# Kernel tuning notes

Measured on AMD Instinct MI355X. Metric: run time of the kernel, lower is better.

## Reference

```python
import jax, jax.numpy as jnp
import numpy as np

B, K, S = 4096, 32, 6          # batch, n_neighbors, n_shifts
QD, H, NH = 512, 384, 6        # query_dim, hidden_dim, n_heads
HD = H // NH                   # head_dim
NR = 20                        # n_residue_types (table has NR+1 rows)
NBR_IN = S + S + 16 + 1 + 1    # neighbor_proj input dim = 30

def gelu(x):
    return jax.nn.gelu(x, approximate=False)

def setup_inputs():
    key = jax.random.key(0)
    ks = iter(jax.random.split(key, 64))
    def nrm(shape, scale=0.05):
        return jax.random.normal(next(ks), shape, dtype=jnp.float32) * scale
    inp = {}
    inp['query_encoding'] = jax.random.normal(next(ks), (B, QD), dtype=jnp.float32)
    inp['query_residue_code'] = jax.random.randint(next(ks), (B,), 0, NR + 1).astype(jnp.int32)
    inp['query_observed_shifts'] = jax.random.normal(next(ks), (B, S), dtype=jnp.float32)
    inp['query_shift_masks'] = (jax.random.uniform(next(ks), (B, S)) < 0.8).astype(jnp.float32)
    inp['retrieved_shifts'] = jax.random.normal(next(ks), (B, K, S), dtype=jnp.float32)
    inp['retrieved_shift_masks'] = jax.random.uniform(next(ks), (B, K, S)) < 0.8
    inp['retrieved_residue_codes'] = jax.random.randint(next(ks), (B, K), 0, NR + 1).astype(jnp.int32)
    inp['retrieved_distances'] = jax.random.uniform(next(ks), (B, K), dtype=jnp.float32)
    inp['retrieved_valid'] = jax.random.uniform(next(ks), (B, K)) < 0.9
    # parameters (buffers + weights). rc_table kept finite (no NaN rows sampled).
    inp['rc_table'] = nrm((NR + 1, S), 1.0)
    inp['W_qp'] = nrm((QD, H)); inp['b_qp'] = jnp.zeros((H,))
    inp['E_res'] = nrm((NR + 1, 16))
    inp['W_np'] = nrm((NBR_IN, H)); inp['b_np'] = jnp.zeros((H,))
    inp['W_aq'] = nrm((H, H)); inp['b_aq'] = jnp.zeros((H,))
    inp['W_ak'] = nrm((H, H)); inp['b_ak'] = jnp.zeros((H,))
    inp['W_av'] = nrm((H, H)); inp['b_av'] = jnp.zeros((H,))
    inp['W_ss1'] = nrm((2 * S, H // 2)); inp['b_ss1'] = jnp.zeros((H // 2,))
    inp['W_ss2'] = nrm((H // 2, NH)); inp['b_ss2'] = jnp.zeros((NH,))
    inp['W_cp1'] = nrm((H, H)); inp['b_cp1'] = jnp.zeros((H,))
    inp['W_cp2'] = nrm((H, H)); inp['b_cp2'] = jnp.zeros((H,))
    inp['W_sw1'] = nrm((H, H)); inp['b_sw1'] = jnp.zeros((H,))
    inp['W_sw2'] = nrm((H, S)); inp['b_sw2'] = jnp.zeros((S,))
    inp['E_trust'] = nrm((NR + 1, 32))
    inp['W_tq'] = nrm((QD, H)); inp['b_tq'] = jnp.zeros((H,))
    inp['W_tc'] = nrm((H + 32 + 4, H)); inp['b_tc'] = jnp.zeros((H,))
    inp['W_tp1'] = nrm((H + 4, H // 2)); inp['b_tp1'] = jnp.zeros((H // 2,))
    inp['W_tp2'] = nrm((H // 2, 1)); inp['b_tp2'] = jnp.zeros((1,))
    inp['shift_scale'] = jnp.ones((S,)); inp['fallback_shift'] = jnp.zeros((S,))
    inp['fallback_context'] = jnp.zeros((H,))
    return inp

def _forward(p):
    eps = 1e-8
    qcode = p['query_residue_code']; rcodes = p['retrieved_residue_codes']
    smask = p['retrieved_shift_masks']; valid = p['retrieved_valid']
    dist = p['retrieved_distances']; rc = p['rc_table']
    # --- RC correction: corrected = RC[query] + (shift - RC[retrieved]) ---
    qidx = jnp.clip(qcode, 0, rc.shape[0] - 1)
    ridx = jnp.clip(rcodes, 0, rc.shape[0] - 1)
    rc_q = rc[qidx][:, None, :]            # (B,1,S)
    rc_r = rc[ridx]                         # (B,K,S)
    corrected = rc_q + (p['retrieved_shifts'] - rc_r)
    rc_valid = (~jnp.isnan(rc_q)) & (~jnp.isnan(rc_r))
    corrected = jnp.where(rc_valid, corrected, p['retrieved_shifts'])
    shifts = jnp.where(smask, corrected, p['retrieved_shifts'])  # (B,K,S)
    any_valid = valid.any(axis=1)                                # (B,)
    same_type = (rcodes == qcode[:, None]).astype(jnp.float32)   # (B,K)
    # --- projections ---
    q = gelu(p['query_encoding'] @ p['W_qp'] + p['b_qp'])        # (B,H)
    res_emb = p['E_res'][rcodes]                                 # (B,K,16)
    nbr = jnp.concatenate([shifts, smask.astype(jnp.float32), res_emb,
                           dist[..., None], same_type[..., None]], axis=-1)
    kv = gelu(nbr @ p['W_np'] + p['b_np'])                       # (B,K,H)
    # --- multi-head cross attention (single query token) ---
    Qh = (q @ p['W_aq'] + p['b_aq']).reshape(B, NH, HD)
    Kh = (kv @ p['W_ak'] + p['b_ak']).reshape(B, K, NH, HD)
    Vh = (kv @ p['W_av'] + p['b_av']).reshape(B, K, NH, HD)
    scores = jnp.einsum('bhd,bkhd->bhk', Qh, Kh) * (HD ** -0.5)  # (B,NH,K)
    sdiff = jnp.concatenate([
        (p['query_observed_shifts'][:, None, :] - shifts) * p['query_shift_masks'][:, None, :],
        jnp.broadcast_to(p['query_shift_masks'][:, None, :], (B, K, S))], axis=-1)
    bias = gelu(sdiff @ p['W_ss1'] + p['b_ss1']) @ p['W_ss2'] + p['b_ss2']  # (B,K,NH)
    scores = scores + jnp.transpose(bias, (0, 2, 1))
    # if nothing valid, unmask slot 0 (matches torch all_masked fixup)
    valid_eff = valid | ((~any_valid)[:, None] & (jnp.arange(K) == 0)[None, :])
    scores = jnp.where(valid_eff[:, None, :], scores, -10000.0)
    w = jax.nn.softmax(scores, axis=-1)
    attn_out = jnp.einsum('bhk,bkhd->bhd', w, Vh).reshape(B, H)
    ctx = gelu(attn_out @ p['W_cp1'] + p['b_cp1']) @ p['W_cp2'] + p['b_cp2']
    ctx = jnp.where(any_valid[:, None], ctx, p['fallback_context'][None, :])
    # --- shift transfer ---
    swb = gelu(attn_out @ p['W_sw1'] + p['b_sw1']) @ p['W_sw2'] + p['b_sw2']  # (B,S)
    weights = dist[..., None] + same_type[..., None] * 0.5 + swb[:, None, :] * 0.1  # (B,K,S)
    valid_mask = valid[..., None] & smask
    weights = jnp.where(valid_mask, weights, -10000.0)
    weights = jax.nn.softmax(weights, axis=1)
    transferred = jnp.sum(weights * shifts, axis=1) * p['shift_scale']
    transferred = jnp.where(any_valid[:, None], transferred, p['fallback_shift'][None, :])
    # --- trust statistics (no grad in original) ---
    vm = valid_mask.astype(jnp.float32)
    cnt = vm.sum(axis=1)                                         # (B,S)
    cov = cnt / (K + eps)
    mean = (shifts * vm).sum(axis=1) / (cnt + eps)
    var = (((shifts - mean[:, None, :]) ** 2) * vm).sum(axis=1) / (cnt + eps)
    var_n = jnp.clip(jnp.log1p(var), 0.0, 5.0) / 5.0
    mdist = (dist[..., None] * vm).sum(axis=1) / (cnt + eps)
    stp = (same_type[..., None] * vm).sum(axis=1) / (cnt + eps)
    per_stats = jax.lax.stop_gradient(jnp.stack([cov, var_n, mdist, stp], axis=-1))  # (B,S,4)
    vf = valid.astype(jnp.float32)
    n_valid = vf.sum(axis=1, keepdims=True) / K
    n_same = (same_type * vf).sum(axis=1, keepdims=True) / K
    dmask = jnp.where(valid, dist, 0.0)
    gmean = dmask.sum(axis=1, keepdims=True) / (vf.sum(axis=1, keepdims=True) + eps)
    gmax = dmask.max(axis=1, keepdims=True)
    gstats = jax.lax.stop_gradient(jnp.concatenate([gmean, gmax, n_valid, n_same], axis=-1))  # (B,4)
    # --- trust head ---
    qre = p['E_trust'][qcode]                                    # (B,32)
    tq = gelu(p['query_encoding'] @ p['W_tq'] + p['b_tq'])
    tc = gelu(jnp.concatenate([tq, qre, gstats], axis=-1) @ p['W_tc'] + p['b_tc'])  # (B,H)
    tin = jnp.concatenate([jnp.broadcast_to(tc[:, None, :], (B, S, H)), per_stats], axis=-1)
    trust = jax.nn.sigmoid(gelu(tin @ p['W_tp1'] + p['b_tp1']) @ p['W_tp2'] + p['b_tp2'])[..., 0]
    return ctx, transferred, trust

def reference(query_encoding, query_residue_code, query_observed_shifts, query_shift_masks,
              retrieved_shifts, retrieved_shift_masks, retrieved_residue_codes,
              retrieved_distances, retrieved_valid, rc_table,
              W_qp, b_qp, E_res, W_np, b_np, W_aq, b_aq, W_ak, b_ak, W_av, b_av,
              W_ss1, b_ss1, W_ss2, b_ss2, W_cp1, b_cp1, W_cp2, b_cp2,
              W_sw1, b_sw1, W_sw2, b_sw2, E_trust, W_tq, b_tq, W_tc, b_tc,
              W_tp1, b_tp1, W_tp2, b_tp2, shift_scale, fallback_shift, fallback_context):
    return _forward(dict(locals()))
```

## Files before the change

kernel.cpp:

```cpp
#include <hip/hip_runtime.h>

typedef unsigned short u16;
typedef unsigned int u32;
typedef __attribute__((ext_vector_type(8))) short bf16x8;
typedef __attribute__((ext_vector_type(4))) float f32x4;

__device__ __forceinline__ float fs(float f) {
    return (f == f && fabsf(f) < 1e30f) ? f : 0.f;
}
__device__ __forceinline__ float fin(float v) {
    return (v == v && fabsf(v) < 1e30f) ? v : 555.0f;
}
__device__ __forceinline__ u16 f2b(float f) {
    union { float f; unsigned int i; } w; w.f = f;
    unsigned int r = w.i + 0x7FFFu + ((w.i >> 16) & 1u);
    return (u16)(r >> 16);
}
__device__ __forceinline__ float b2f(u16 b) {
    union { unsigned int i; float f; } w; w.i = ((unsigned int)b) << 16;
    return w.f;
}
__device__ __forceinline__ float gelu_f(float x) {
    return 0.5f * x * (1.0f + erff(x * 0.70710678118654752440f));
}

__global__ void fill_kernel(float* __restrict__ out, int n, float val) {
    int i = blockIdx.x * 256 + threadIdx.x;
    if (i < n) out[i] = val;
}

struct CvtSrcs { const float* p[13]; };

__global__ void k_cvt_all(CvtSrcs sp, u16* __restrict__ w) {
    int id = blockIdx.x * 256 + threadIdx.x;
    if (id >= 3634304) return;
    if (id < 2097152) { w[id] = f2b(fs(sp.p[0][id])); return; }
    if (id >= 2637824 && id < 2785280) { w[id] = f2b(fs(sp.p[4][id - 2637824])); return; }
    const float* src; int local, K, N, Kp;
    if (id < 2293760)      { src = sp.p[1];  local = id - 2097152; K = 512; N = 384; Kp = 512; }
    else if (id < 2490368) { src = sp.p[2];  local = id - 2293760; K = 512; N = 384; Kp = 512; }
    else if (id < 2637824) { src = sp.p[3];  local = id - 2490368; K = 384; N = 384; Kp = 384; }
    else if (id < 2932736) { src = sp.p[5];  local = id - 2785280; K = 384; N = 384; Kp = 384; }
    else if (id < 3080192) { src = sp.p[6];  local = id - 2932736; K = 384; N = 384; Kp = 384; }
    else if (id < 3227648) { src = sp.p[7];  local = id - 3080192; K = 384; N = 384; Kp = 384; }
    else if (id < 3375104) { src = sp.p[8];  local = id - 3227648; K = 384; N = 384; Kp = 384; }
    else if (id < 3547136) { src = sp.p[9];  local = id - 3375104; K = 420; N = 384; Kp = 448; }
    else if (id < 3620864) { src = sp.p[10]; local = id - 3547136; K = 384; N = 192; Kp = 384; }
    else if (id < 3633152) { src = sp.p[11]; local = id - 3620864; K = 30;  N = 384; Kp = 32;  }
    else                   { src = sp.p[12]; local = id - 3633152; K = 192; N = 6;   Kp = 192; }
    int n = local / Kp, k = local - n * Kp;
    w[id] = (k < K) ? f2b(fs(src[(size_t)k * N + n])) : (u16)0;
}

__global__ void k_prep(const float* __restrict__ qobs, const float* __restrict__ qmask,
                       const float* __restrict__ rshift, const int* __restrict__ rsmask,
                       const int* __restrict__ qcode, const int* __restrict__ rcodes,
                       const float* __restrict__ rdist, const float* __restrict__ rc_table,
                       const float* __restrict__ E_res,
                       float* __restrict__ nbr, float* __restrict__ sdiff, int NBc)
{
    int gk = blockIdx.x * 256 + threadIdx.x;
    if (gk >= NBc) return;
    int b = gk >> 5;
    int qc = qcode[b], rc = rcodes[gk];
    int qi = min(max(qc, 0), 20), ri = min(max(rc, 0), 20);
    float dist = fs(rdist[gk]);
    float same = (rc == qc) ? 1.f : 0.f;
    float* nr = nbr + (size_t)gk * 30;
    float* sd = sdiff + (size_t)gk * 12;
    for (int s = 0; s < 6; s++) {
        float rs = fs(rshift[gk * 6 + s]);
        bool m = rsmask[gk * 6 + s] != 0;
        float rq = rc_table[qi * 6 + s];
        float rr = rc_table[ri * 6 + s];
        bool rcv = (rq == rq) && (rr == rr) && fabsf(rq) < 1e30f && fabsf(rr) < 1e30f;
        float sh = (m && rcv) ? (rq + rs - rr) : rs;
        nr[s] = sh;
        nr[6 + s] = m ? 1.f : 0.f;
        float qm = fs(qmask[b * 6 + s]);
        sd[s] = (fs(qobs[b * 6 + s]) - sh) * qm;
        sd[6 + s] = qm;
    }
    for (int j = 0; j < 16; j++) nr[12 + j] = fs(E_res[ri * 16 + j]);
    nr[28] = dist;
    nr[29] = same;
}

__global__ void k_stats_w(const float* __restrict__ nbr, const int* __restrict__ rvalid,
                          float* __restrict__ pst, float* __restrict__ gst,
                          float* __restrict__ anyv, int BCc)
{
    int wid = (blockIdx.x * 256 + threadIdx.x) >> 6;
    int lane = threadIdx.x & 63;
    if (wid >= BCc * 4) return;
    int b = wid >> 2, sub = wid & 3;
    if (sub < 3) {
        int s = sub * 2 + (lane >> 5), k = lane & 31;
        const float* nr = nbr + (size_t)(b * 32 + k) * 30;
        float vf = (rvalid[b * 32 + k] != 0) ? 1.f : 0.f;
        float vm = vf * nr[6 + s];
        float shv = nr[s], dist = nr[28], same = nr[29];
        float cnt = vm, msum = shv * vm, mdist = dist * vm, mst = same * vm;
#pragma unroll
        for (int m = 1; m <= 16; m <<= 1) {
            cnt += __shfl_xor(cnt, m);
            msum += __shfl_xor(msum, m);
            mdist += __shfl_xor(mdist, m);
            mst += __shfl_xor(mst, m);
        }
        float inv = 1.f / (cnt + 1e-8f);
        float mean = msum * inv;
        float dv = shv - mean;
        float var = dv * dv * vm;
#pragma unroll
        for (int m = 1; m <= 16; m <<= 1) var += __shfl_xor(var, m);
        var *= inv;
        if (k == 0) {
            float* p = pst + (size_t)b * 24 + s * 4;
            p[0] = cnt * (1.f / 32.f);
            p[1] = fminf(fmaxf(log1pf(var), 0.f), 5.f) * 0.2f;
            p[2] = mdist * inv;
            p[3] = mst * inv;
        }
    } else {
        int k = lane & 31;
        float svf = 0.f, sdm = 0.f, mdm = -1e30f, ssm = 0.f;
        if (lane < 32) {
            const float* nr = nbr + (size_t)(b * 32 + k) * 30;
            float vf = (rvalid[b * 32 + k] != 0) ? 1.f : 0.f;
            float dm = vf * nr[28];
            svf = vf; sdm = dm; mdm = dm; ssm = vf * nr[29];
        }
#pragma unroll
        for (int m = 1; m <= 32; m <<= 1) {
            svf += __shfl_xor(svf, m);
            sdm += __shfl_xor(sdm, m);
            mdm = fmaxf(mdm, __shfl_xor(mdm, m));
            ssm += __shfl_xor(ssm, m);
        }
        if (lane == 0) {
            float* g = gst + (size_t)b * 4;
            g[0] = sdm / (svf + 1e-8f);
            g[1] = mdm;
            g[2] = svf * (1.f / 32.f);
            g[3] = ssm * (1.f / 32.f);
            anyv[b] = (svf > 0.f) ? 1.f : 0.f;
        }
    }
}

template <int ACT, bool OUTF, bool OUTB>
__device__ __forceinline__ void gemm_body128(
    const u16* __restrict__ A, int lda,
    const u16* __restrict__ BT, int ldb,
    const float* __restrict__ bias, const float* __restrict__ bias1,
    float* __restrict__ Cf, u16* __restrict__ Cb, int ldc,
    int K, int m0, int n0)
{
    __shared__ u16 As[128 * 72];
    __shared__ u16 Bs[64 * 72];
    const int t = threadIdx.x;
    const int lane = t & 63, wave = t >> 6;
    const int wm = (wave & 1) << 6, wn = (wave >> 1) << 5;
    const int frm = lane & 15, frq = lane >> 4;
    const int r0 = t >> 3, c0 = (t & 7) << 3;
    const f32x4 z = {0.f, 0.f, 0.f, 0.f};
    f32x4 acc[4][2] = {{z, z}, {z, z}, {z, z}, {z, z}};
    for (int k0 = 0; k0 < K; k0 += 64) {
#pragma unroll
        for (int i = 0; i < 4; i++)
            *(bf16x8*)&As[(r0 + 32 * i) * 72 + c0] =
                *(const bf16x8*)&A[(size_t)(m0 + r0 + 32 * i) * lda + k0 + c0];
#pragma unroll
        for (int i = 0; i < 2; i++)
            *(bf16x8*)&Bs[(r0 + 32 * i) * 72 + c0] =
                *(const bf16x8*)&BT[(size_t)(n0 + r0 + 32 * i) * ldb + k0 + c0];
        __syncthreads();
#pragma unroll
        for (int kk = 0; kk < 2; kk++) {
            const int fo = (kk << 5) + (frq << 3);
            bf16x8 b0 = *(const bf16x8*)&Bs[(wn + frm) * 72 + fo];
            bf16x8 b1 = *(const bf16x8*)&Bs[(wn + 16 + frm) * 72 + fo];
#pragma unroll
            for (int mi = 0; mi < 4; mi++) {
                bf16x8 a = *(const bf16x8*)&As[(wm + (mi << 4) + frm) * 72 + fo];
                acc[mi][0] = __builtin_amdgcn_mfma_f32_16x16x32_bf16(a, b0, acc[mi][0], 0, 0, 0);
                acc[mi][1] = __builtin_amdgcn_mfma_f32_16x16x32_bf16(a, b1, acc[mi][1], 0, 0, 0);
            }
        }
        __syncthreads();
    }
#pragma unroll
    for (int mi = 0; mi < 4; mi++) {
#pragma unroll
        for (int ni = 0; ni < 2; ni++) {
            int col = n0 + wn + (ni << 4) + frm;
            float bv = 0.f;
            if (bias) {
                if (bias1 && col >= 384) bv = fs(bias1[col - 384]);
                else bv = fs(bias[col]);
            }
#pragma unroll
            for (int r = 0; r < 4; r++) {
                int row = m0 + wm + (mi << 4) + (frq << 2) + r;
                float v = acc[mi][ni][r] + bv;
                if (ACT == 1) v = gelu_f(v);
                if (OUTF) Cf[(size_t)row * ldc + col] = v;
                if (OUTB) Cb[(size_t)row * ldc + col] = f2b(v);
            }
        }
    }
}

template <int ACT, bool OUTF, bool OUTB>
__global__ __launch_bounds__(256) void k_gemm_bb(
    const u16* __restrict__ A, int lda, const u16* __restrict__ BT, int ldb,
    const float* __restrict__ bias, float* __restrict__ Cf, u16* __restrict__ Cb,
    int ldc, int K)
{
    gemm_body128<ACT, OUTF, OUTB>(A, lda, BT, ldb, bias, nullptr, Cf, Cb, ldc, K,
                                  blockIdx.y << 7, blockIdx.x << 6);
}

template <int ACT>
__global__ __launch_bounds__(256) void k_gemm_bb2(
    const u16* __restrict__ A, int lda, const u16* __restrict__ BT, int ldb,
    const float* __restrict__ bias0, const float* __restrict__ bias1,
    u16* __restrict__ Cb, int ldc, int K)
{
    gemm_body128<ACT, false, true>(A, lda, BT, ldb, bias0, bias1, nullptr, Cb, ldc, K,
                                   blockIdx.y << 7, blockIdx.x << 6);
}

__global__ __launch_bounds__(256) void k_gemm_ctx(
    const u16* __restrict__ A, int lda, const u16* __restrict__ BT, int ldb,
    const float* __restrict__ bias, const float* __restrict__ anyv,
    const float* __restrict__ fctx, float* __restrict__ outp, int ldc, int K)
{
    __shared__ u16 As[128 * 72];
    __shared__ u16 Bs[64 * 72];
    const int t = threadIdx.x;
    const int lane = t & 63, wave = t >> 6;
    const int m0 = blockIdx.y << 7, n0 = blockIdx.x << 6;
    const int wm = (wave & 1) << 6, wn = (wave >> 1) << 5;
    const int frm = lane & 15, frq = lane >> 4;
    const int r0 = t >> 3, c0 = (t & 7) << 3;
    const f32x4 z = {0.f, 0.f, 0.f, 0.f};
    f32x4 acc[4][2] = {{z, z}, {z, z}, {z, z}, {z, z}};
    for (int k0 = 0; k0 < K; k0 += 64) {
#pragma unroll
        for (int i = 0; i < 4; i++)
            *(bf16x8*)&As[(r0 + 32 * i) * 72 + c0] =
                *(const bf16x8*)&A[(size_t)(m0 + r0 + 32 * i) * lda + k0 + c0];
#pragma unroll
        for (int i = 0; i < 2; i++)
            *(bf16x8*)&Bs[(r0 + 32 * i) * 72 + c0] =
                *(const bf16x8*)&BT[(size_t)(n0 + r0 + 32 * i) * ldb + k0 + c0];
        __syncthreads();
#pragma unroll
        for (int kk = 0; kk < 2; kk++) {
            const int fo = (kk << 5) + (frq << 3);
            bf16x8 b0 = *(const bf16x8*)&Bs[(wn + frm) * 72 + fo];
            bf16x8 b1 = *(const bf16x8*)&Bs[(wn + 16 + frm) * 72 + fo];
#pragma unroll
            for (int mi = 0; mi < 4; mi++) {
                bf16x8 a = *(const bf16x8*)&As[(wm + (mi << 4) + frm) * 72 + fo];
                acc[mi][0] = __builtin_amdgcn_mfma_f32_16x16x32_bf16(a, b0, acc[mi][0], 0, 0, 0);
                acc[mi][1] = __builtin_amdgcn_mfma_f32_16x16x32_bf16(a, b1, acc[mi][1], 0, 0, 0);
            }
        }
        __syncthreads();
    }
#pragma unroll
    for (int mi = 0; mi < 4; mi++) {
#pragma unroll
        for (int ni = 0; ni < 2; ni++) {
            int col = n0 + wn + (ni << 4) + frm;
            float bv = fs(bias[col]);
            float fv = fs(fctx[col]);
#pragma unroll
            for (int r = 0; r < 4; r++) {
                int row = m0 + wm + (mi << 4) + (frq << 2) + r;
                float v = acc[mi][ni][r] + bv;
                v = (anyv[row] > 0.f) ? v : fv;
                outp[(size_t)row * ldc + col] = fin(v);
            }
        }
    }
}

__global__ __launch_bounds__(256) void k_gemm_tc(
    const u16* __restrict__ qtqb, const int* __restrict__ qcode,
    const float* __restrict__ Etr, const float* __restrict__ gst,
    const u16* __restrict__ BT, const float* __restrict__ bias,
    u16* __restrict__ Cb)
{
    __shared__ u16 As[128 * 72];
    __shared__ u16 Bs[64 * 72];
    const int t = threadIdx.x;
    const int lane = t & 63, wave = t >> 6;
    const int m0 = blockIdx.y << 7, n0 = blockIdx.x << 6;
    const int wm = (wave & 1) << 6, wn = (wave >> 1) << 5;
    const int frm = lane & 15, frq = lane >> 4;
    const int r0 = t >> 3, c0 = (t & 7) << 3;
    const f32x4 z = {0.f, 0.f, 0.f, 0.f};
    f32x4 acc[4][2] = {{z, z}, {z, z}, {z, z}, {z, z}};
    for (int k0 = 0; k0 < 448; k0 += 64) {
        if (k0 < 384) {
#pragma unroll
            for (int i = 0; i < 4; i++)
                *(bf16x8*)&As[(r0 + 32 * i) * 72 + c0] =
                    *(const bf16x8*)&qtqb[(size_t)(m0 + r0 + 32 * i) * 768 + 384 + k0 + c0];
        } else {
#pragma unroll
            for (int i = 0; i < 4; i++) {
                int row = m0 + r0 + 32 * i;
                int qi = min(max(qcode[row], 0), 20);
#pragma unroll
                for (int j = 0; j < 8; j++) {
                    int col = k0 + c0 + j;
                    u16 v;
                    if (col < 416) v = f2b(fs(Etr[qi * 32 + (col - 384)]));
                    else if (col < 420) v = f2b(gst[(size_t)row * 4 + (col - 416)]);
                    else v = (u16)0;
                    As[(r0 + 32 * i) * 72 + c0 + j] = v;
                }
            }
        }
#pragma unroll
        for (int i = 0; i < 2; i++)
            *(bf16x8*)&Bs[(r0 + 32 * i) * 72 + c0] =
                *(const bf16x8*)&BT[(size_t)(n0 + r0 + 32 * i) * 448 + k0 + c0];
        __syncthreads();
#pragma unroll
        for (int kk = 0; kk < 2; kk++) {
            const int fo = (kk << 5) + (frq << 3);
            bf16x8 b0 = *(const bf16x8*)&Bs[(wn + frm) * 72 + fo];
            bf16x8 b1 = *(const bf16x8*)&Bs[(wn + 16 + frm) * 72 + fo];
#pragma unroll
            for (int mi = 0; mi < 4; mi++) {
                bf16x8 a = *(const bf16x8*)&As[(wm + (mi << 4) + frm) * 72 + fo];
                acc[mi][0] = __builtin_amdgcn_mfma_f32_16x16x32_bf16(a, b0, acc[mi][0], 0, 0, 0);
                acc[mi][1] = __builtin_amdgcn_mfma_f32_16x16x32_bf16(a, b1, acc[mi][1], 0, 0, 0);
            }
        }
        __syncthreads();
    }
#pragma unroll
    for (int mi = 0; mi < 4; mi++) {
#pragma unroll
        for (int ni = 0; ni < 2; ni++) {
            int col = n0 + wn + (ni << 4) + frm;
            float bv = fs(bias[col]);
#pragma unroll
            for (int r = 0; r < 4; r++) {
                int row = m0 + wm + (mi << 4) + (frq << 2) + r;
                Cb[(size_t)row * 384 + col] = f2b(gelu_f(acc[mi][ni][r] + bv));
            }
        }
    }
}

__global__ __launch_bounds__(256) void k_qp_loop(
    const u16* __restrict__ Qhb, const u16* __restrict__ WakB,
    const float* __restrict__ bak, u16* __restrict__ Qpb, float* __restrict__ qkb)
{
    __shared__ u16 As[64 * 72];
    __shared__ u16 Bs[64 * 72];
    const int t = threadIdx.x;
    const int lane = t & 63, wave = t >> 6;
    const int m0 = blockIdx.x << 6, hd = blockIdx.y;
    const int wm = (wave & 1) << 5, wn = (wave >> 1) << 5;
    const int frm = lane & 15, frq = lane >> 4;
    const int r0 = t >> 3, c0 = (t & 7) << 3;
    const f32x4 z = {0.f, 0.f, 0.f, 0.f};
    *(bf16x8*)&As[r0 * 72 + c0]        = *(const bf16x8*)&Qhb[(size_t)(m0 + r0) * 384 + hd * 64 + c0];
    *(bf16x8*)&As[(r0 + 32) * 72 + c0] = *(const bf16x8*)&Qhb[(size_t)(m0 + r0 + 32) * 384 + hd * 64 + c0];
    __syncthreads();
    {
        int r = t >> 2, p = t & 3;
        float acc = 0.f;
#pragma unroll
        for (int i = 0; i < 16; i++) {
            int d = p * 16 + i;
            acc += b2f(As[r * 72 + d]) * fs(bak[hd * 64 + d]);
        }
        acc += __shfl_xor(acc, 1);
        acc += __shfl_xor(acc, 2);
        if (p == 0) qkb[(m0 + r) * 6 + hd] = acc;
    }
    for (int nt = 0; nt < 6; nt++) {
        *(bf16x8*)&Bs[r0 * 72 + c0]        = *(const bf16x8*)&WakB[(size_t)(nt * 64 + r0) * 384 + hd * 64 + c0];
        *(bf16x8*)&Bs[(r0 + 32) * 72 + c0] = *(const bf16x8*)&WakB[(size_t)(nt * 64 + r0 + 32) * 384 + hd * 64 + c0];
        __syncthreads();
        f32x4 acc[2][2] = {{z, z}, {z, z}};
#pragma unroll
        for (int kk = 0; kk < 2; kk++) {
            const int fo = (kk << 5) + (frq << 3);
            bf16x8 a0 = *(const bf16x8*)&As[(wm + frm) * 72 + fo];
            bf16x8 a1 = *(const bf16x8*)&As[(wm + 16 + frm) * 72 + fo];
            bf16x8 b0 = *(const bf16x8*)&Bs[(wn + frm) * 72 + fo];
            bf16x8 b1 = *(const bf16x8*)&Bs[(wn + 16 + frm) * 72 + fo];
            acc[0][0] = __builtin_amdgcn_mfma_f32_16x16x32_bf16(a0, b0, acc[0][0], 0, 0, 0);
            acc[0][1] = __builtin_amdgcn_mfma_f32_16x16x32_bf16(a0, b1, acc[0][1], 0, 0, 0);
            acc[1][0] = __builtin_amdgcn_mfma_f32_16x16x32_bf16(a1, b0, acc[1][0], 0, 0, 0);
            acc[1][1] = __builtin_amdgcn_mfma_f32_16x16x32_bf16(a1, b1, acc[1][1], 0, 0, 0);
        }
#pragma unroll
        for (int mi = 0; mi < 2; mi++) {
#pragma unroll
            for (int ni = 0; ni < 2; ni++) {
                int col = nt * 64 + wn + (ni << 4) + frm;
#pragma unroll
                for (int r = 0; r < 4; r++) {
                    int row = m0 + wm + (mi << 4) + (frq << 2) + r;
                    Qpb[(size_t)row * 2304 + hd * 384 + col] = f2b(acc[mi][ni][r]);
                }
            }
        }
        __syncthreads();
    }
}

__global__ __launch_bounds__(256) void k_attnout_bb(
    const u16* __restrict__ vmsb, const u16* __restrict__ WavT,
    const float* __restrict__ bav, u16* __restrict__ attnb)
{
    int hd = blockIdx.x;
    gemm_body128<0, false, true>(vmsb + hd * 384, 2304, WavT + (size_t)hd * 64 * 384, 384,
                                 bav + hd * 64, nullptr, nullptr, attnb + hd * 64, 384, 384,
                                 blockIdx.y << 7, 0);
}

__global__ __launch_bounds__(192) void k_mlpbias(
    const float* __restrict__ sdiff, const float* __restrict__ Wss1,
    const float* __restrict__ bss1, const u16* __restrict__ Wss2T,
    const float* __restrict__ bss2, float* __restrict__ bias_s)
{
    __shared__ float sdS[32 * 12];
    __shared__ u16 hidSb[32 * 200];
    const int b = blockIdx.x;
    const int t = threadIdx.x;
    for (int i = t; i < 384; i += 192) sdS[i] = sdiff[(size_t)b * 384 + i];
    __syncthreads();
    {
        float w[12];
#pragma unroll
        for (int j = 0; j < 12; j++) w[j] = fs(Wss1[j * 192 + t]);
        float b1 = fs(bss1[t]);
        for (int k = 0; k < 32; k++) {
            float acc = b1;
#pragma unroll
            for (int j = 0; j < 12; j++) acc += sdS[k * 12 + j] * w[j];
            hidSb[k * 200 + t] = f2b(gelu_f(acc));
        }
    }
    __syncthreads();
    if (t < 64) {
        const int frm = t & 15, frq = t >> 4;
        const f32x4 z = {0.f, 0.f, 0.f, 0.f};
        f32x4 acc0 = z, acc1 = z;
        const u16* bt = Wss2T + (frm < 6 ? frm : 0) * 192;
#pragma unroll
        for (int ks = 0; ks < 6; ks++) {
            bf16x8 bf = *(const bf16x8*)&bt[ks * 32 + (frq << 3)];
            bf16x8 a0 = *(const bf16x8*)&hidSb[frm * 200 + ks * 32 + (frq << 3)];
            bf16x8 a1 = *(const bf16x8*)&hidSb[(16 + frm) * 200 + ks * 32 + (frq << 3)];
            acc0 = __builtin_amdgcn_mfma_f32_16x16x32_bf16(a0, bf, acc0, 0, 0, 0);
            acc1 = __builtin_amdgcn_mfma_f32_16x16x32_bf16(a1, bf, acc1, 0, 0, 0);
        }
        if (frm < 6) {
            float bb = fs(bss2[frm]);
#pragma unroll
            for (int r = 0; r < 4; r++) {
                int kk = (frq << 2) + r;
                bias_s[(size_t)(b * 32 + kk) * 6 + frm] = acc0[r] + bb;
                bias_s[(size_t)(b * 32 + kk + 16) * 6 + frm] = acc1[r] + bb;
            }
        }
    }
}

__global__ __launch_bounds__(384) void k_attnblk(
    const float* __restrict__ nbr, const u16* __restrict__ WnpT,
    const float* __restrict__ bnp, const u16* __restrict__ Qpb,
    const float* __restrict__ qkb, const float* __restrict__ bias_s,
    const int* __restrict__ rvalid, const float* __restrict__ anyv,
    u16* __restrict__ vmsb)
{
    __shared__ u16 kvsb[32 * 392];
    __shared__ u16 qSb[6 * 392];
    __shared__ float wsx[192];
    __shared__ float uSf[512];
    u16* aS = (u16*)uSf;
    float* sS = uSf;
    const int b = blockIdx.x;
    const int t = threadIdx.x;
    const int lane = t & 63, wave = t >> 6;
    const int frm = lane & 15, frq = lane >> 4;
    for (int i = t; i < 1152; i += 384) {
        int h = i / 192, k2 = i - h * 192;
        ((u32*)qSb)[h * 196 + k2] = ((const u32*)(Qpb + (size_t)b * 2304))[i];
    }
    {
        const float* nr = nbr + (size_t)b * 960;
        for (int i = t; i < 1024; i += 384) {
            int r = i >> 5, cc = i & 31;
            aS[r * 32 + cc] = (cc < 30) ? f2b(nr[r * 30 + cc]) : (u16)0;
        }
    }
    __syncthreads();
    {
        bf16x8 a0 = *(const bf16x8*)&aS[frm * 32 + (frq << 3)];
        bf16x8 a1 = *(const bf16x8*)&aS[(16 + frm) * 32 + (frq << 3)];
        const f32x4 z = {0.f, 0.f, 0.f, 0.f};
        f32x4 acc0[4] = {z, z, z, z};
        f32x4 acc1[4] = {z, z, z, z};
#pragma unroll
        for (int ct = 0; ct < 4; ct++) {
            int col = (wave << 6) + (ct << 4) + frm;
            bf16x8 bf = *(const bf16x8*)&WnpT[col * 32 + (frq << 3)];
            acc0[ct] = __builtin_amdgcn_mfma_f32_16x16x32_bf16(a0, bf, acc0[ct], 0, 0, 0);
            acc1[ct] = __builtin_amdgcn_mfma_f32_16x16x32_bf16(a1, bf, acc1[ct], 0, 0, 0);
        }
#pragma unroll
        for (int ct = 0; ct < 4; ct++) {
            int col = (wave << 6) + (ct << 4) + frm;
            float bb = fs(bnp[col]);
#pragma unroll
            for (int r = 0; r < 4; r++) {
                int row0 = (frq << 2) + r;
                kvsb[row0 * 392 + col] = f2b(gelu_f(acc0[ct][r] + bb));
                kvsb[(row0 + 16) * 392 + col] = f2b(gelu_f(acc1[ct][r] + bb));
            }
        }
    }
    __syncthreads();
    if (wave < 2) {
        f32x4 accs = {0.f, 0.f, 0.f, 0.f};
#pragma unroll
        for (int ks = 0; ks < 12; ks++) {
            bf16x8 af = *(const bf16x8*)&kvsb[((wave << 4) + frm) * 392 + (ks << 5) + (frq << 3)];
            int hh = (frm < 6) ? frm : 0;
            bf16x8 bf = *(const bf16x8*)&qSb[hh * 392 + (ks << 5) + (frq << 3)];
            accs = __builtin_amdgcn_mfma_f32_16x16x32_bf16(af, bf, accs, 0, 0, 0);
        }
        if (frm < 6) {
#pragma unroll
            for (int r = 0; r < 4; r++)
                sS[((wave << 4) + (frq << 2) + r) * 8 + frm] = accs[r];
        }
    }
    __syncthreads();
    if (t < 192) {
        int h = t >> 5, k = t & 31;
        float s = (sS[k * 8 + h] + qkb[b * 6 + h]) * 0.125f
                + bias_s[(size_t)(b * 32 + k) * 6 + h];
        bool ve = (rvalid[b * 32 + k] != 0) || (anyv[b] == 0.f && k == 0);
        s = ve ? s : -10000.f;
        float mx = s;
        mx = fmaxf(mx, __shfl_xor(mx, 1));
        mx = fmaxf(mx, __shfl_xor(mx, 2));
        mx = fmaxf(mx, __shfl_xor(mx, 4));
        mx = fmaxf(mx, __shfl_xor(mx, 8));
        mx = fmaxf(mx, __shfl_xor(mx, 16));
        float e = expf(s - mx);
        float sum = e;
        sum += __shfl_xor(sum, 1);
        sum += __shfl_xor(sum, 2);
        sum += __shfl_xor(sum, 4);
        sum += __shfl_xor(sum, 8);
        sum += __shfl_xor(sum, 16);
        wsx[h * 32 + k] = e / sum;
    }
    __syncthreads();
    {
        float a0 = 0.f, a1 = 0.f, a2 = 0.f, a3 = 0.f, a4 = 0.f, a5 = 0.f;
        for (int k = 0; k < 32; k++) {
            float kvv = b2f(kvsb[k * 392 + t]);
            a0 += wsx[k] * kvv;
            a1 += wsx[32 + k] * kvv;
            a2 += wsx[64 + k] * kvv;
            a3 += wsx[96 + k] * kvv;
            a4 += wsx[128 + k] * kvv;
            a5 += wsx[160 + k] * kvv;
        }
        u16* vp = vmsb + (size_t)b * 2304;
        vp[t] = f2b(a0);
        vp[384 + t] = f2b(a1);
        vp[768 + t] = f2b(a2);
        vp[1152 + t] = f2b(a3);
        vp[1536 + t] = f2b(a4);
        vp[1920 + t] = f2b(a5);
    }
}

__global__ void k_swb_w(const u16* __restrict__ hs1b, const float* __restrict__ Wsw2,
                        const float* __restrict__ bsw2, float* __restrict__ swb, int BCc)
{
    int wid = (blockIdx.x * 256 + threadIdx.x) >> 6;
    int lane = threadIdx.x & 63;
    if (wid >= BCc * 6) return;
    int b = wid / 6, s = wid - b * 6;
    float acc = 0.f;
#pragma unroll
    for (int i = 0; i < 6; i++) {
        int n = lane + 64 * i;
        acc += b2f(hs1b[(size_t)b * 768 + 384 + n]) * fs(Wsw2[n * 6 + s]);
    }
#pragma unroll
    for (int m = 1; m <= 32; m <<= 1) acc += __shfl_xor(acc, m);
    if (lane == 0) swb[b * 6 + s] = acc + fs(bsw2[s]);
}

__global__ void k_tail_w(const float* __restrict__ tcp, const float* __restrict__ pst,
                         const float* __restrict__ Wtp1, const float* __restrict__ Wtp2,
                         const float* __restrict__ btp2, float* __restrict__ outT,
                         const float* __restrict__ nbr, const int* __restrict__ rsmask,
                         const int* __restrict__ rvalid, const float* __restrict__ swb,
                         const float* __restrict__ anyv, const float* __restrict__ sscale,
                         const float* __restrict__ fshift, float* __restrict__ outX, int BCc)
{
    int wid = (blockIdx.x * 256 + threadIdx.x) >> 6;
    int lane = threadIdx.x & 63;
    if (wid >= BCc * 9) return;
    int b = wid / 9, sub = wid - b * 9;
    if (sub < 6) {
        int s = sub;
        const float* ps = pst + (size_t)b * 24 + s * 4;
        float p0 = ps[0], p1 = ps[1], p2 = ps[2], p3 = ps[3];
        float acc = 0.f;
#pragma unroll
        for (int i = 0; i < 3; i++) {
            int j = lane + 64 * i;
            float pre = tcp[(size_t)b * 192 + j];
            pre += p0 * fs(Wtp1[(size_t)384 * 192 + j]);
            pre += p1 * fs(Wtp1[(size_t)385 * 192 + j]);
            pre += p2 * fs(Wtp1[(size_t)386 * 192 + j]);
            pre += p3 * fs(Wtp1[(size_t)387 * 192 + j]);
            acc += gelu_f(pre) * fs(Wtp2[j]);
        }
#pragma unroll
        for (int m = 1; m <= 32; m <<= 1) acc += __shfl_xor(acc, m);
        if (lane == 0) {
            float tv = 1.f / (1.f + expf(-(acc + fs(btp2[0]))));
            outT[b * 6 + s] = fin(tv);
        }
    } else {
        int s2 = sub - 6;
        int s = s2 * 2 + (lane >> 5), k = lane & 31;
        if (anyv[b] <= 0.f) {
            if (k == 0) outX[b * 6 + s] = fin(fs(fshift[s]));
            return;
        }
        int gk = b * 32 + k;
        const float* nr = nbr + (size_t)gk * 30;
        float wb = swb[b * 6 + s] * 0.1f;
        bool m = (rvalid[gk] != 0) && (rsmask[gk * 6 + s] != 0);
        float wv = m ? (nr[28] + nr[29] * 0.5f + wb) : -10000.f;
        float mx = wv;
#pragma unroll
        for (int mm = 1; mm <= 16; mm <<= 1) mx = fmaxf(mx, __shfl_xor(mx, mm));
        float e = expf(wv - mx);
        float num = e * nr[s], den = e;
#pragma unroll
        for (int mm = 1; mm <= 16; mm <<= 1) {
            num += __shfl_xor(num, mm);
            den += __shfl_xor(den, mm);
        }
        if (k == 0) outX[b * 6 + s] = fin((num / den) * fs(sscale[s]));
    }
}

#define L1(total) <<<((total) + 255) / 256, 256, 0, stream>>>
#define LW(nwaves) <<<(((nwaves) * 64) + 255) / 256, 256, 0, stream>>>

extern "C" void kernel_launch(void* const* d_in, const int* in_sizes, int n_in,
                              void* d_out, int out_size, void* d_ws, size_t ws_size,
                              hipStream_t stream)
{
    float* out = (float*)d_out;

    static const int EXP[45] = {
        2097152, 4096, 24576, 24576, 786432, 786432, 131072, 131072, 131072, 126,
        196608, 384, 336, 11520, 384, 147456, 384, 147456, 384, 147456, 384,
        2304, 192, 1152, 6, 147456, 384, 147456, 384, 147456, 384, 2304, 6,
        672, 196608, 384, 161280, 384, 74496, 192, 192, 1, 6, 6, 384
    };
    if (n_in != 45) {
        fill_kernel L1(out_size)(out, out_size, 580.0f);
        return;
    }
    for (int i = 0; i < 45; i++) {
        if (in_sizes[i] != EXP[i]) {
            fill_kernel L1(out_size)(out, out_size, 600.0f + 4.0f * i);
            return;
        }
    }

    const float* i_qe    = (const float*)d_in[0];
    const int*   i_qcode = (const int*)d_in[1];
    const float* i_qobs  = (const float*)d_in[2];
    const float* i_qmask = (const float*)d_in[3];
    const float* i_rshift= (const float*)d_in[4];
    const int*   i_rsmask= (const int*)d_in[5];
    const int*   i_rcodes= (const int*)d_in[6];
    const float* i_rdist = (const float*)d_in[7];
    const int*   i_rvalid= (const int*)d_in[8];
    const float* i_rc    = (const float*)d_in[9];
    const float* i_Wqp   = (const float*)d_in[10];
    const float* i_bqp   = (const float*)d_in[11];
    const float* i_Eres  = (const float*)d_in[12];
    const float* i_Wnp   = (const float*)d_in[13];
    const float* i_bnp   = (const float*)d_in[14];
    const float* i_Waq   = (const float*)d_in[15];
    const float* i_baq   = (const float*)d_in[16];
    const float* i_Wak   = (const float*)d_in[17];
    const float* i_bak   = (const float*)d_in[18];
    const float* i_Wav   = (const float*)d_in[19];
    const float* i_bav   = (const float*)d_in[20];
    const float* i_Wss1  = (const float*)d_in[21];
    const float* i_bss1  = (const float*)d_in[22];
    const float* i_Wss2  = (const float*)d_in[23];
    const float* i_bss2  = (const float*)d_in[24];
    const float* i_Wcp1  = (const float*)d_in[25];
    const float* i_bcp1  = (const float*)d_in[26];
    const float* i_Wcp2  = (const float*)d_in[27];
    const float* i_bcp2  = (const float*)d_in[28];
    const float* i_Wsw1  = (const float*)d_in[29];
    const float* i_bsw1  = (const float*)d_in[30];
    const float* i_Wsw2  = (const float*)d_in[31];
    const float* i_bsw2  = (const float*)d_in[32];
    const float* i_Etr   = (const float*)d_in[33];
    const float* i_Wtq   = (const float*)d_in[34];
    const float* i_btq   = (const float*)d_in[35];
    const float* i_Wtc   = (const float*)d_in[36];
    const float* i_btc   = (const float*)d_in[37];
    const float* i_Wtp1  = (const float*)d_in[38];
    const float* i_btp1  = (const float*)d_in[39];
    const float* i_Wtp2  = (const float*)d_in[40];
    const float* i_btp2  = (const float*)d_in[41];
    const float* i_sscale= (const float*)d_in[42];
    const float* i_fshift= (const float*)d_in[43];
    const float* i_fctx  = (const float*)d_in[44];

    auto layoutBytes = [](int bc) -> size_t {
        auto al = [](size_t x) { return (x + 255) & ~(size_t)255; };
        size_t off = 0;
        off += al(3634304ull * 2);
        size_t nb = (size_t)bc * 32;
        off += al(nb * 30 * 4) + al(nb * 12 * 4) + al(nb * 6 * 4);
        off += al((size_t)bc * 192 * 4);
        off += al((size_t)bc * 2304 * 2) * 2;
        off += al((size_t)bc * 768 * 2) * 2;
        off += al((size_t)bc * 384 * 2) * 3;
        off += al((size_t)bc * 6 * 4) * 2 + al((size_t)bc * 24 * 4)
             + al((size_t)bc * 4 * 4) + al((size_t)bc * 4);
        return off;
    };
    const int cand[6] = {4096, 2048, 1024, 512, 256, 128};
    int BCc = 128;
    for (int i = 0; i < 6; i++) {
        if (layoutBytes(cand[i]) <= ws_size) { BCc = cand[i]; break; }
    }
    const int NBc = BCc * 32;

    char* wsb = (char*)d_ws;
    size_t off = 0;
    auto allocB = [&](size_t bytes) -> void* {
        void* p = (void*)(wsb + off);
        off = (off + bytes + 255) & ~(size_t)255;
        return p;
    };
    u16* wsW = (u16*)allocB(3634304ull * 2);
    u16* qeb   = wsW;
    u16* WqtqT = wsW + 2097152;
    u16* WaqT  = wsW + 2490368;
    u16* WakB  = wsW + 2637824;
    u16* WavT  = wsW + 2785280;
    u16* Wcp2T = wsW + 2932736;
    u16* Whs1T = wsW + 3080192;
    u16* WtcT  = wsW + 3375104;
    u16* Wtp1T = wsW + 3547136;
    u16* WnpT  = wsW + 3620864;
    u16* Wss2T = wsW + 3633152;
    float* nbr   = (float*)allocB((size_t)NBc * 30 * 4);
    float* sdiff = (float*)allocB((size_t)NBc * 12 * 4);
    float* bias_s= (float*)allocB((size_t)NBc * 6 * 4);
    float* tcpf  = (float*)allocB((size_t)BCc * 192 * 4);
    u16*   Qpb   = (u16*)allocB((size_t)BCc * 2304 * 2);
    u16*   vmsb  = (u16*)allocB((size_t)BCc * 2304 * 2);
    u16*   qtqb  = (u16*)allocB((size_t)BCc * 768 * 2);
    u16*   hs1b  = (u16*)allocB((size_t)BCc * 768 * 2);
    u16*   Qhb   = (u16*)allocB((size_t)BCc * 384 * 2);
    u16*   attnb = (u16*)allocB((size_t)BCc * 384 * 2);
    u16*   tcb   = (u16*)allocB((size_t)BCc * 384 * 2);
    float* swbf  = (float*)allocB((size_t)BCc * 6 * 4);
    float* qkbf  = (float*)allocB((size_t)BCc * 6 * 4);
    float* pstf  = (float*)allocB((size_t)BCc * 24 * 4);
    float* gstf  = (float*)allocB((size_t)BCc * 4 * 4);
    float* anyf  = (float*)allocB((size_t)BCc * 4);

    if (off > ws_size) {
        fill_kernel L1(out_size)(out, out_size, 1000.0f);
        return;
    }

    CvtSrcs sp;
    sp.p[0] = i_qe;  sp.p[1] = i_Wqp;  sp.p[2] = i_Wtq;  sp.p[3] = i_Waq;
    sp.p[4] = i_Wak; sp.p[5] = i_Wav;  sp.p[6] = i_Wcp2; sp.p[7] = i_Wcp1;
    sp.p[8] = i_Wsw1; sp.p[9] = i_Wtc; sp.p[10] = i_Wtp1; sp.p[11] = i_Wnp;
    sp.p[12] = i_Wss2;
    k_cvt_all L1(3634304)(sp, wsW);

    for (int c = 0; c < 4096 / BCc; c++) {
        const size_t B0 = (size_t)c * BCc;
        const int MB = BCc / 128;
        const dim3 g6(6, MB), g3(3, MB), g12(12, MB), gao(6, MB);
        const dim3 gqp(BCc / 64, 6);
        k_prep L1(NBc)(i_qobs + B0 * 6, i_qmask + B0 * 6, i_rshift + B0 * 192,
                       i_rsmask + B0 * 192, i_qcode + B0, i_rcodes + B0 * 32,
                       i_rdist + B0 * 32, i_rc, i_Eres, nbr, sdiff, NBc);
        k_stats_w LW(BCc * 4)(nbr, i_rvalid + B0 * 32, pstf, gstf, anyf, BCc);
        k_mlpbias<<<BCc, 192, 0, stream>>>(sdiff, i_Wss1, i_bss1, Wss2T, i_bss2, bias_s);
        k_gemm_bb2<1><<<g12, 256, 0, stream>>>(
            qeb + B0 * 512, 512, WqtqT, 512, i_bqp, i_btq, qtqb, 768, 512);
        k_gemm_bb<0, false, true><<<g6, 256, 0, stream>>>(
            qtqb, 768, WaqT, 384, i_baq, nullptr, Qhb, 384, 384);
        k_qp_loop<<<gqp, 256, 0, stream>>>(Qhb, WakB, i_bak, Qpb, qkbf);
        k_attnblk<<<BCc, 384, 0, stream>>>(nbr, WnpT, i_bnp, Qpb, qkbf, bias_s,
                                           i_rvalid + B0 * 32, anyf, vmsb);
        k_attnout_bb<<<gao, 256, 0, stream>>>(vmsb, WavT, i_bav, attnb);
        k_gemm_bb2<1><<<g12, 256, 0, stream>>>(
            attnb, 384, Whs1T, 384, i_bcp1, i_bsw1, hs1b, 768, 384);
        k_gemm_ctx<<<g6, 256, 0, stream>>>(
            hs1b, 768, Wcp2T, 384, i_bcp2, anyf, i_fctx, out + B0 * 384, 384, 384);
        k_swb_w LW(BCc * 6)(hs1b, i_Wsw2, i_bsw2, swbf, BCc);
        k_gemm_tc<<<g6, 256, 0, stream>>>(
            qtqb, i_qcode + B0, i_Etr, gstf, WtcT, i_btc, tcb);
        k_gemm_bb<0, true, false><<<g3, 256, 0, stream>>>(
            tcb, 384, Wtp1T, 384, i_btp1, tcpf, nullptr, 192, 384);
        k_tail_w LW(BCc * 9)(tcpf, pstf, i_Wtp1, i_Wtp2, i_btp2,
                             out + (size_t)4096 * 390 + B0 * 6,
                             nbr, i_rsmask + B0 * 192, i_rvalid + B0 * 32, swbf, anyf,
                             i_sscale, i_fshift, out + (size_t)4096 * 384 + B0 * 6, BCc);
    }
}
```

Before: 396.8 us.

## Fuse shift-similarity MLP bias into attention block kernel

Removes the separate k_mlpbias kernel and the sdiff/bias_s global buffers. The shift-difference features, the first MLP layer (now done with MFMA on a bf16-transposed Wss1) and the second layer are computed inside k_attnblk using shared memory, with waves 2-3 doing the second layer in parallel with the score computation. This saves a kernel launch and global round trips per chunk. In exchange it adds shared memory and extra work to the attention kernel, which may lower occupancy, and it rounds the first-layer inputs to bf16.

```diff
diff --git a/kernel.cpp b/kernel.cpp
--- a/kernel.cpp
+++ b/kernel.cpp
@@ -29,11 +29,11 @@
     if (i < n) out[i] = val;
 }
 
-struct CvtSrcs { const float* p[13]; };
+struct CvtSrcs { const float* p[14]; };
 
 __global__ void k_cvt_all(CvtSrcs sp, u16* __restrict__ w) {
     int id = blockIdx.x * 256 + threadIdx.x;
-    if (id >= 3634304) return;
+    if (id >= 3640448) return;
     if (id < 2097152) { w[id] = f2b(fs(sp.p[0][id])); return; }
     if (id >= 2637824 && id < 2785280) { w[id] = f2b(fs(sp.p[4][id - 2637824])); return; }
     const float* src; int local, K, N, Kp;
@@ -47,17 +47,17 @@
     else if (id < 3547136) { src = sp.p[9];  local = id - 3375104; K = 420; N = 384; Kp = 448; }
     else if (id < 3620864) { src = sp.p[10]; local = id - 3547136; K = 384; N = 192; Kp = 384; }
     else if (id < 3633152) { src = sp.p[11]; local = id - 3620864; K = 30;  N = 384; Kp = 32;  }
-    else                   { src = sp.p[12]; local = id - 3633152; K = 192; N = 6;   Kp = 192; }
+    else if (id < 3634304) { src = sp.p[12]; local = id - 3633152; K = 192; N = 6;   Kp = 192; }
+    else                   { src = sp.p[13]; local = id - 3634304; K = 12;  N = 192; Kp = 32;  }
     int n = local / Kp, k = local - n * Kp;
     w[id] = (k < K) ? f2b(fs(src[(size_t)k * N + n])) : (u16)0;
 }
 
-__global__ void k_prep(const float* __restrict__ qobs, const float* __restrict__ qmask,
-                       const float* __restrict__ rshift, const int* __restrict__ rsmask,
+__global__ void k_prep(const float* __restrict__ rshift, const int* __restrict__ rsmask,
                        const int* __restrict__ qcode, const int* __restrict__ rcodes,
                        const float* __restrict__ rdist, const float* __restrict__ rc_table,
                        const float* __restrict__ E_res,
-                       float* __restrict__ nbr, float* __restrict__ sdiff, int NBc)
+                       float* __restrict__ nbr, int NBc)
 {
     int gk = blockIdx.x * 256 + threadIdx.x;
     if (gk >= NBc) return;
@@ -67,7 +67,6 @@
     float dist = fs(rdist[gk]);
     float same = (rc == qc) ? 1.f : 0.f;
     float* nr = nbr + (size_t)gk * 30;
-    float* sd = sdiff + (size_t)gk * 12;
     for (int s = 0; s < 6; s++) {
         float rs = fs(rshift[gk * 6 + s]);
         bool m = rsmask[gk * 6 + s] != 0;
@@ -77,9 +76,6 @@
         float sh = (m && rcv) ? (rq + rs - rr) : rs;
         nr[s] = sh;
         nr[6 + s] = m ? 1.f : 0.f;
-        float qm = fs(qmask[b * 6 + s]);
-        sd[s] = (fs(qobs[b * 6 + s]) - sh) * qm;
-        sd[6 + s] = qm;
     }
     for (int j = 0; j < 16; j++) nr[12 + j] = fs(E_res[ri * 16 + j]);
     nr[28] = dist;
@@ -432,65 +428,22 @@
                                  blockIdx.y << 7, 0);
 }
 
-__global__ __launch_bounds__(192) void k_mlpbias(
-    const float* __restrict__ sdiff, const float* __restrict__ Wss1,
-    const float* __restrict__ bss1, const u16* __restrict__ Wss2T,
-    const float* __restrict__ bss2, float* __restrict__ bias_s)
-{
-    __shared__ float sdS[32 * 12];
-    __shared__ u16 hidSb[32 * 200];
-    const int b = blockIdx.x;
-    const int t = threadIdx.x;
-    for (int i = t; i < 384; i += 192) sdS[i] = sdiff[(size_t)b * 384 + i];
-    __syncthreads();
-    {
-        float w[12];
-#pragma unroll
-        for (int j = 0; j < 12; j++) w[j] = fs(Wss1[j * 192 + t]);
-        float b1 = fs(bss1[t]);
-        for (int k = 0; k < 32; k++) {
-            float acc = b1;
-#pragma unroll
-            for (int j = 0; j < 12; j++) acc += sdS[k * 12 + j] * w[j];
-            hidSb[k * 200 + t] = f2b(gelu_f(acc));
-        }
-    }
-    __syncthreads();
-    if (t < 64) {
-        const int frm = t & 15, frq = t >> 4;
-        const f32x4 z = {0.f, 0.f, 0.f, 0.f};
-        f32x4 acc0 = z, acc1 = z;
-        const u16* bt = Wss2T + (frm < 6 ? frm : 0) * 192;
-#pragma unroll
-        for (int ks = 0; ks < 6; ks++) {
-            bf16x8 bf = *(const bf16x8*)&bt[ks * 32 + (frq << 3)];
-            bf16x8 a0 = *(const bf16x8*)&hidSb[frm * 200 + ks * 32 + (frq << 3)];
-            bf16x8 a1 = *(const bf16x8*)&hidSb[(16 + frm) * 200 + ks * 32 + (frq << 3)];
-            acc0 = __builtin_amdgcn_mfma_f32_16x16x32_bf16(a0, bf, acc0, 0, 0, 0);
-            acc1 = __builtin_amdgcn_mfma_f32_16x16x32_bf16(a1, bf, acc1, 0, 0, 0);
-        }
-        if (frm < 6) {
-            float bb = fs(bss2[frm]);
-#pragma unroll
-            for (int r = 0; r < 4; r++) {
-                int kk = (frq << 2) + r;
-                bias_s[(size_t)(b * 32 + kk) * 6 + frm] = acc0[r] + bb;
-                bias_s[(size_t)(b * 32 + kk + 16) * 6 + frm] = acc1[r] + bb;
-            }
-        }
-    }
-}
-
 __global__ __launch_bounds__(384) void k_attnblk(
     const float* __restrict__ nbr, const u16* __restrict__ WnpT,
     const float* __restrict__ bnp, const u16* __restrict__ Qpb,
-    const float* __restrict__ qkb, const float* __restrict__ bias_s,
+    const float* __restrict__ qkb,
+    const float* __restrict__ qobs, const float* __restrict__ qmask,
+    const u16* __restrict__ Wss1T, const float* __restrict__ bss1,
+    const u16* __restrict__ Wss2T, const float* __restrict__ bss2,
     const int* __restrict__ rvalid, const float* __restrict__ anyv,
     u16* __restrict__ vmsb)
 {
     __shared__ u16 kvsb[32 * 392];
     __shared__ u16 qSb[6 * 392];
+    __shared__ u16 hidSb[32 * 200];
+    __shared__ u16 sdS[32 * 32];
     __shared__ float wsx[192];
+    __shared__ float bsS[32 * 8];
     __shared__ float uSf[512];
     u16* aS = (u16*)uSf;
     float* sS = uSf;
@@ -508,6 +461,17 @@
             int r = i >> 5, cc = i & 31;
             aS[r * 32 + cc] = (cc < 30) ? f2b(nr[r * 30 + cc]) : (u16)0;
         }
+        if (t < 32) {
+            const float* nr2 = nr + t * 30;
+#pragma unroll
+            for (int s = 0; s < 6; s++) {
+                float qm = fs(qmask[b * 6 + s]);
+                sdS[t * 32 + s] = f2b((fs(qobs[b * 6 + s]) - nr2[s]) * qm);
+                sdS[t * 32 + 6 + s] = f2b(qm);
+            }
+#pragma unroll
+            for (int j = 12; j < 32; j++) sdS[t * 32 + j] = (u16)0;
+        }
     }
     __syncthreads();
     {
@@ -534,6 +498,22 @@
                 kvsb[(row0 + 16) * 392 + col] = f2b(gelu_f(acc1[ct][r] + bb));
             }
         }
+        bf16x8 sa0 = *(const bf16x8*)&sdS[frm * 32 + (frq << 3)];
+        bf16x8 sa1 = *(const bf16x8*)&sdS[(16 + frm) * 32 + (frq << 3)];
+#pragma unroll
+        for (int ct = 0; ct < 2; ct++) {
+            int col = (wave << 5) + (ct << 4) + frm;
+            bf16x8 bf = *(const bf16x8*)&Wss1T[col * 32 + (frq << 3)];
+            f32x4 d0 = __builtin_amdgcn_mfma_f32_16x16x32_bf16(sa0, bf, z, 0, 0, 0);
+            f32x4 d1 = __builtin_amdgcn_mfma_f32_16x16x32_bf16(sa1, bf, z, 0, 0, 0);
+            float bb = fs(bss1[col]);
+#pragma unroll
+            for (int r = 0; r < 4; r++) {
+                int k0r = (frq << 2) + r;
+                hidSb[k0r * 200 + col] = f2b(gelu_f(d0[r] + bb));
+                hidSb[(k0r + 16) * 200 + col] = f2b(gelu_f(d1[r] + bb));
+            }
+        }
     }
     __syncthreads();
     if (wave < 2) {
@@ -550,12 +530,26 @@
             for (int r = 0; r < 4; r++)
                 sS[((wave << 4) + (frq << 2) + r) * 8 + frm] = accs[r];
         }
+    } else if (wave < 4) {
+        int w2 = wave - 2;
+        f32x4 accb = {0.f, 0.f, 0.f, 0.f};
+#pragma unroll
+        for (int ks = 0; ks < 6; ks++) {
+            bf16x8 a = *(const bf16x8*)&hidSb[((w2 << 4) + frm) * 200 + (ks << 5) + (frq << 3)];
+            bf16x8 bf = *(const bf16x8*)&Wss2T[(frm < 6 ? frm : 0) * 192 + (ks << 5) + (frq << 3)];
+            accb = __builtin_amdgcn_mfma_f32_16x16x32_bf16(a, bf, accb, 0, 0, 0);
+        }
+        if (frm < 6) {
+            float bb = fs(bss2[frm]);
+#pragma unroll
+            for (int r = 0; r < 4; r++)
+                bsS[((w2 << 4) + (frq << 2) + r) * 8 + frm] = accb[r] + bb;
+        }
     }
     __syncthreads();
     if (t < 192) {
         int h = t >> 5, k = t & 31;
-        float s = (sS[k * 8 + h] + qkb[b * 6 + h]) * 0.125f
-                + bias_s[(size_t)(b * 32 + k) * 6 + h];
+        float s = (sS[k * 8 + h] + qkb[b * 6 + h]) * 0.125f + bsS[k * 8 + h];
         bool ve = (rvalid[b * 32 + k] != 0) || (anyv[b] == 0.f && k == 0);
         s = ve ? s : -10000.f;
         float mx = s;
@@ -747,9 +741,9 @@
     auto layoutBytes = [](int bc) -> size_t {
         auto al = [](size_t x) { return (x + 255) & ~(size_t)255; };
         size_t off = 0;
-        off += al(3634304ull * 2);
+        off += al(3640448ull * 2);
         size_t nb = (size_t)bc * 32;
-        off += al(nb * 30 * 4) + al(nb * 12 * 4) + al(nb * 6 * 4);
+        off += al(nb * 30 * 4);
         off += al((size_t)bc * 192 * 4);
         off += al((size_t)bc * 2304 * 2) * 2;
         off += al((size_t)bc * 768 * 2) * 2;
@@ -772,7 +766,7 @@
         off = (off + bytes + 255) & ~(size_t)255;
         return p;
     };
-    u16* wsW = (u16*)allocB(3634304ull * 2);
+    u16* wsW = (u16*)allocB(3640448ull * 2);
     u16* qeb   = wsW;
     u16* WqtqT = wsW + 2097152;
     u16* WaqT  = wsW + 2490368;
@@ -784,9 +778,8 @@
     u16* Wtp1T = wsW + 3547136;
     u16* WnpT  = wsW + 3620864;
     u16* Wss2T = wsW + 3633152;
+    u16* Wss1T = wsW + 3634304;
     float* nbr   = (float*)allocB((size_t)NBc * 30 * 4);
-    float* sdiff = (float*)allocB((size_t)NBc * 12 * 4);
-    float* bias_s= (float*)allocB((size_t)NBc * 6 * 4);
     float* tcpf  = (float*)allocB((size_t)BCc * 192 * 4);
     u16*   Qpb   = (u16*)allocB((size_t)BCc * 2304 * 2);
     u16*   vmsb  = (u16*)allocB((size_t)BCc * 2304 * 2);
@@ -810,25 +803,25 @@
     sp.p[0] = i_qe;  sp.p[1] = i_Wqp;  sp.p[2] = i_Wtq;  sp.p[3] = i_Waq;
     sp.p[4] = i_Wak; sp.p[5] = i_Wav;  sp.p[6] = i_Wcp2; sp.p[7] = i_Wcp1;
     sp.p[8] = i_Wsw1; sp.p[9] = i_Wtc; sp.p[10] = i_Wtp1; sp.p[11] = i_Wnp;
-    sp.p[12] = i_Wss2;
-    k_cvt_all L1(3634304)(sp, wsW);
+    sp.p[12] = i_Wss2; sp.p[13] = i_Wss1;
+    k_cvt_all L1(3640448)(sp, wsW);
 
     for (int c = 0; c < 4096 / BCc; c++) {
         const size_t B0 = (size_t)c * BCc;
         const int MB = BCc / 128;
         const dim3 g6(6, MB), g3(3, MB), g12(12, MB), gao(6, MB);
         const dim3 gqp(BCc / 64, 6);
-        k_prep L1(NBc)(i_qobs + B0 * 6, i_qmask + B0 * 6, i_rshift + B0 * 192,
-                       i_rsmask + B0 * 192, i_qcode + B0, i_rcodes + B0 * 32,
-                       i_rdist + B0 * 32, i_rc, i_Eres, nbr, sdiff, NBc);
+        k_prep L1(NBc)(i_rshift + B0 * 192, i_rsmask + B0 * 192, i_qcode + B0,
+                       i_rcodes + B0 * 32, i_rdist + B0 * 32, i_rc, i_Eres, nbr, NBc);
         k_stats_w LW(BCc * 4)(nbr, i_rvalid + B0 * 32, pstf, gstf, anyf, BCc);
-        k_mlpbias<<<BCc, 192, 0, stream>>>(sdiff, i_Wss1, i_bss1, Wss2T, i_bss2, bias_s);
         k_gemm_bb2<1><<<g12, 256, 0, stream>>>(
             qeb + B0 * 512, 512, WqtqT, 512, i_bqp, i_btq, qtqb, 768, 512);
         k_gemm_bb<0, false, true><<<g6, 256, 0, stream>>>(
             qtqb, 768, WaqT, 384, i_baq, nullptr, Qhb, 384, 384);
         k_qp_loop<<<gqp, 256, 0, stream>>>(Qhb, WakB, i_bak, Qpb, qkbf);
-        k_attnblk<<<BCc, 384, 0, stream>>>(nbr, WnpT, i_bnp, Qpb, qkbf, bias_s,
+        k_attnblk<<<BCc, 384, 0, stream>>>(nbr, WnpT, i_bnp, Qpb, qkbf,
+                                           i_qobs + B0 * 6, i_qmask + B0 * 6,
+                                           Wss1T, i_bss1, Wss2T, i_bss2,
                                            i_rvalid + B0 * 32, anyf, vmsb);
         k_attnout_bb<<<gao, 256, 0, stream>>>(vmsb, WavT, i_bav, attnb);
         k_gemm_bb2<1><<<g12, 256, 0, stream>>>(
```

After: 394.2 us. Within noise of the previous version (-0.7%).
